# Performance work log

Measured on AMD Instinct MI355X. Metric: run time of the kernel, lower is better.

Reference implementation:

```python
import jax, jax.numpy as jnp
import numpy as np

N_NODES = 100000
N_EDGES = 1600000
IN_SIZE = 512
HID_SIZE = 256
OUT_SIZE = 40
K_STEPS = 10
ALPHA = 0.1


def setup_inputs() -> dict:
    key = jax.random.key(0)
    ks = jax.random.split(key, 8)
    features = jax.random.normal(ks[0], (N_NODES, IN_SIZE), dtype=jnp.float32)
    src = jax.random.randint(ks[1], (N_EDGES,), 0, N_NODES, dtype=jnp.int64)
    dst = jax.random.randint(ks[2], (N_EDGES,), 0, N_NODES, dtype=jnp.int64)
    # MLP params (Kaiming-ish scale)
    W1 = jax.random.normal(ks[3], (IN_SIZE, HID_SIZE), dtype=jnp.float32) / np.sqrt(IN_SIZE)
    b1 = jnp.zeros((HID_SIZE,), dtype=jnp.float32)
    W2 = jax.random.normal(ks[4], (HID_SIZE, OUT_SIZE), dtype=jnp.float32) / np.sqrt(HID_SIZE)
    b2 = jnp.zeros((OUT_SIZE,), dtype=jnp.float32)
    return {"features": features, "src": src, "dst": dst,
            "W1": W1, "b1": b1, "W2": W2, "b2": b2}


def reference(features, src, dst, W1, b1, W2, b2):
    # --- MLP encoder (dropout is identity in eval mode) ---
    h = jax.nn.relu(features @ W1 + b1)
    h = h @ W2 + b2  # [N, out_size]

    # --- Symmetric normalization (DGL APPNPConv, edge_weight=None) ---
    ones_e = jnp.ones((src.shape[0],), dtype=h.dtype)
    deg_out = jax.ops.segment_sum(ones_e, src, num_segments=N_NODES)
    deg_in = jax.ops.segment_sum(ones_e, dst, num_segments=N_NODES)
    norm_src = jnp.power(jnp.clip(deg_out, 1.0), -0.5)[:, None]  # D_out^{-1/2}
    norm_dst = jnp.power(jnp.clip(deg_in, 1.0), -0.5)[:, None]   # D_in^{-1/2}

    # --- k=10 APPNP propagation: h <- (1-a) * D^{-1/2} A D^{-1/2} h + a * h0 ---
    h0 = h

    def step(h, _):
        msg = (h * norm_src)[src]                                  # gather [E, out]
        agg = jax.ops.segment_sum(msg, dst, num_segments=N_NODES)  # scatter-add
        h = (1.0 - ALPHA) * (agg * norm_dst) + ALPHA * h0
        return h, None

    h, _ = jax.lax.scan(step, h, None, length=K_STEPS)
    return h
```

## Files before the change

### kernel.cpp

```cpp
#include <hip/hip_runtime.h>

#define N_NODES 100000
#define N_EDGES 1600000
#define IN_SIZE 512
#define HID_SIZE 256
#define OUT_SIZE 40
#define K_STEPS 10
#define ALPHA 0.1f
#define NP 100096

#define NCH 250
#define CH_E 6400
#define NBUK 391
#define NRS 8
#define HRS 12544
#define NCS 16
#define CS_E 100000

typedef _Float16 half8 __attribute__((ext_vector_type(8)));
typedef _Float16 half4 __attribute__((ext_vector_type(4)));
typedef float f32x4 __attribute__((ext_vector_type(4)));

struct __align__(8) Entry { int s; int d; };

__device__ inline void gld_lds16(const void* g, void* l) {
    __builtin_amdgcn_global_load_lds(
        (const __attribute__((address_space(1))) void*)g,
        (__attribute__((address_space(3))) void*)l,
        16, 0, 0);
}

__global__ __launch_bounds__(512) void hist_pass(const int* __restrict__ dst,
                                                 int* __restrict__ cnt) {
    __shared__ int h[NBUK];
    const int t = threadIdx.x, c = blockIdx.x;
    for (int j = t; j < NBUK; j += 512) h[j] = 0;
    __syncthreads();
    const int4* d4 = (const int4*)(dst + c * CH_E);
    for (int i = t; i < CH_E / 4; i += 512) {
        const int4 v = d4[i];
        atomicAdd(&h[v.x >> 8], 1);
        atomicAdd(&h[v.y >> 8], 1);
        atomicAdd(&h[v.z >> 8], 1);
        atomicAdd(&h[v.w >> 8], 1);
    }
    __syncthreads();
    for (int j = t; j < NBUK; j += 512) cnt[c * NBUK + j] = h[j];
}

__global__ __launch_bounds__(512) void bucket_scan(const int* __restrict__ cnt,
                                                   int* __restrict__ off,
                                                   int* __restrict__ boff) {
    __shared__ int tot[512];
    const int b = threadIdx.x;
    int s = 0;
    if (b < NBUK)
        for (int c = 0; c < NCH; ++c) s += cnt[c * NBUK + b];
    tot[b] = s;
    __syncthreads();
    for (int o = 1; o < 512; o <<= 1) {
        const int v = (b >= o) ? tot[b - o] : 0;
        __syncthreads();
        tot[b] += v;
        __syncthreads();
    }
    if (b < NBUK) {
        int run = tot[b] - s;
        boff[b] = run;
        for (int c = 0; c < NCH; ++c) { off[c * NBUK + b] = run; run += cnt[c * NBUK + b]; }
        if (b == NBUK - 1) boff[NBUK] = tot[b];
    }
}

__global__ __launch_bounds__(512) void scatter_pass(const int* __restrict__ src,
                                                    const int* __restrict__ dst,
                                                    const int* __restrict__ off,
                                                    Entry* __restrict__ ebuf) {
    __shared__ int cur[NBUK];
    const int t = threadIdx.x, c = blockIdx.x;
    for (int j = t; j < NBUK; j += 512) cur[j] = off[c * NBUK + j];
    __syncthreads();
    const int4* s4 = (const int4*)(src + c * CH_E);
    const int4* d4 = (const int4*)(dst + c * CH_E);
    for (int i = t; i < CH_E / 4; i += 512) {
        const int4 sv = s4[i];
        const int4 dv = d4[i];
        Entry e;
        int p;
        p = atomicAdd(&cur[dv.x >> 8], 1); e.s = sv.x; e.d = dv.x; ebuf[p] = e;
        p = atomicAdd(&cur[dv.y >> 8], 1); e.s = sv.y; e.d = dv.y; ebuf[p] = e;
        p = atomicAdd(&cur[dv.z >> 8], 1); e.s = sv.z; e.d = dv.z; ebuf[p] = e;
        p = atomicAdd(&cur[dv.w >> 8], 1); e.s = sv.w; e.d = dv.w; ebuf[p] = e;
    }
}

__global__ __launch_bounds__(256) void bucket_csr(const Entry* __restrict__ ebuf,
                                                  const int* __restrict__ boff,
                                                  int* __restrict__ rowp,
                                                  float* __restrict__ ndst,
                                                  int* __restrict__ csr) {
    __shared__ int hist[256];
    __shared__ int pref[256];
    __shared__ int cur[256];
    const int t = threadIdx.x, b = blockIdx.x;
    const int beg = boff[b], end = boff[b + 1];
    hist[t] = 0;
    __syncthreads();
    for (int i = beg + t; i < end; i += 256)
        atomicAdd(&hist[ebuf[i].d & 255], 1);
    __syncthreads();
    const int h = hist[t];
    pref[t] = h;
    __syncthreads();
    for (int o = 1; o < 256; o <<= 1) {
        const int v = (t >= o) ? pref[t - o] : 0;
        __syncthreads();
        pref[t] += v;
        __syncthreads();
    }
    const int val = beg + pref[t] - h;
    const int n = (b << 8) + t;
    if (n <= N_NODES) rowp[n] = val;
    if (n < N_NODES) ndst[n] = 1.0f / sqrtf((float)max(h, 1));
    cur[t] = val;
    __syncthreads();
    for (int i = beg + t; i < end; i += 256) {
        const Entry e = ebuf[i];
        const int pos = atomicAdd(&cur[e.d & 255], 1);
        csr[pos] = e.s;
    }
}

__global__ __launch_bounds__(512) void degsrc_part(const int* __restrict__ src,
                                                   int* __restrict__ partial) {
    __shared__ int h[HRS];
    const int t = threadIdx.x;
    const int r = blockIdx.x & (NRS - 1);
    const int c = blockIdx.x >> 3;
    const int base = r * HRS;
    for (int j = t; j < HRS; j += 512) h[j] = 0;
    __syncthreads();
    const int4* s4 = (const int4*)(src + (size_t)c * CS_E);
    for (int i = t; i < CS_E / 4; i += 512) {
        const int4 v = s4[i];
        unsigned u;
        u = (unsigned)(v.x - base); if (u < HRS) atomicAdd(&h[u], 1);
        u = (unsigned)(v.y - base); if (u < HRS) atomicAdd(&h[u], 1);
        u = (unsigned)(v.z - base); if (u < HRS) atomicAdd(&h[u], 1);
        u = (unsigned)(v.w - base); if (u < HRS) atomicAdd(&h[u], 1);
    }
    __syncthreads();
    for (int j = t; j < HRS; j += 512) partial[(size_t)c * (NRS * HRS) + base + j] = h[j];
}

__global__ __launch_bounds__(256) void nsrc_reduce(const int* __restrict__ partial,
                                                   float* __restrict__ nsrc) {
    const int n = blockIdx.x * 256 + threadIdx.x;
    int s = 0;
#pragma unroll
    for (int c = 0; c < NCS; ++c) s += partial[(size_t)c * (NRS * HRS) + n];
    if (n < N_NODES) nsrc[n] = 1.0f / sqrtf((float)max(s, 1));
}

__global__ __launch_bounds__(256) void prep_w1tp(const float* __restrict__ W1,
                                                 unsigned short* __restrict__ w1tp) {
    int idx = blockIdx.x * 256 + threadIdx.x;
    if (idx < IN_SIZE * HID_SIZE) {
        const int kt  = idx >> 14;
        const int p   = idx & 16383;
        const int n   = p >> 6;
        const int off = p & 63;
        const int j   = off & 7;
        const int ch  = (off >> 3) ^ (n & 7);
        const int kg  = kt * 64 + ch * 8 + j;
        _Float16 h = (_Float16)W1[(size_t)kg * HID_SIZE + n];
        w1tp[idx] = *(unsigned short*)&h;
    }
}

__global__ __launch_bounds__(512) void gemm1_f16(const float* __restrict__ X,
                                                 const unsigned short* __restrict__ w1tp,
                                                 const float* __restrict__ b1,
                                                 _Float16* __restrict__ h1t) {
    __shared__ __align__(16) _Float16 sA[128 * 64];
    __shared__ __align__(16) _Float16 sB[256 * 64];

    const int t    = threadIdx.x;
    const int lane = t & 63;
    const int w    = t >> 6;
    const int wr   = w >> 2;
    const int wc   = w & 3;
    const int n0   = blockIdx.x * 128;

    f32x4 acc[4][4];
#pragma unroll
    for (int i = 0; i < 4; ++i)
#pragma unroll
        for (int j = 0; j < 4; ++j) acc[i][j] = (f32x4)0.f;

    const int lo = lane & 15;
    const int hi = lane >> 4;
    const int l7 = lane & 7;

    for (int kk = 0; kk < IN_SIZE; kk += 64) {
        __syncthreads();
        {
            const unsigned short* gsrc = w1tp + ((size_t)(kk >> 6) << 14);
#pragma unroll
            for (int i = 0; i < 4; ++i) {
                const int c = t + i * 512;
                gld_lds16(gsrc + c * 8, &sB[c * 8]);
            }
        }
#pragma unroll
        for (int i = 0; i < 2; ++i) {
            int id  = t + i * 512;
            int row = id >> 3;
            int ch  = id & 7;
            int gr  = n0 + row;
            float4 x0 = make_float4(0.f, 0.f, 0.f, 0.f), x1 = x0;
            if (gr < N_NODES) {
                const float* p = X + (size_t)gr * IN_SIZE + kk + ch * 8;
                x0 = ((const float4*)p)[0];
                x1 = ((const float4*)p)[1];
            }
            half8 hv;
            hv[0] = (_Float16)x0.x; hv[1] = (_Float16)x0.y;
            hv[2] = (_Float16)x0.z; hv[3] = (_Float16)x0.w;
            hv[4] = (_Float16)x1.x; hv[5] = (_Float16)x1.y;
            hv[6] = (_Float16)x1.z; hv[7] = (_Float16)x1.w;
            *(half8*)&sA[row * 64 + ((ch ^ (row & 7)) << 3)] = hv;
        }
        __syncthreads();
#pragma unroll
        for (int s = 0; s < 2; ++s) {
            const int chs = ((s * 4 + hi) ^ l7) << 3;
            half8 af[4], bf[4];
#pragma unroll
            for (int f = 0; f < 4; ++f)
                af[f] = *(const half8*)&sA[(wr * 64 + f * 16 + lo) * 64 + chs];
#pragma unroll
            for (int f = 0; f < 4; ++f)
                bf[f] = *(const half8*)&sB[(wc * 64 + f * 16 + lo) * 64 + chs];
#pragma unroll
            for (int fi = 0; fi < 4; ++fi)
#pragma unroll
                for (int fj = 0; fj < 4; ++fj)
                    acc[fi][fj] = __builtin_amdgcn_mfma_f32_16x16x32_f16(
                        af[fi], bf[fj], acc[fi][fj], 0, 0, 0);
        }
    }

    float b1v[4];
#pragma unroll
    for (int fj = 0; fj < 4; ++fj) b1v[fj] = b1[wc * 64 + fj * 16 + lo];
#pragma unroll
    for (int fi = 0; fi < 4; ++fi) {
        const int nb = n0 + wr * 64 + fi * 16 + hi * 4;
#pragma unroll
        for (int fj = 0; fj < 4; ++fj) {
            const int c = wc * 64 + fj * 16 + lo;
            half4 hv;
#pragma unroll
            for (int r = 0; r < 4; ++r)
                hv[r] = (_Float16)fmaxf(acc[fi][fj][r] + b1v[fj], 0.f);
            *(half4*)(h1t + (size_t)c * NP + nb) = hv;
        }
    }
}

__global__ __launch_bounds__(256) void gemm2t(const _Float16* __restrict__ h1t,
                                              const float* __restrict__ W2,
                                              const float* __restrict__ b2,
                                              float* __restrict__ h0) {
    __shared__ float sW2[HID_SIZE * OUT_SIZE];
    const int t = threadIdx.x;
    const int n = blockIdx.x * 256 + t;
    for (int i = t; i < HID_SIZE * OUT_SIZE; i += 256) sW2[i] = W2[i];
    __syncthreads();

    float acc[OUT_SIZE];
#pragma unroll
    for (int o = 0; o < OUT_SIZE; ++o) acc[o] = b2[o];

    const _Float16* hp = h1t + n;
#pragma unroll 4
    for (int c = 0; c < HID_SIZE; ++c) {
        const float hv = (float)hp[(size_t)c * NP];
        const float* wrow = &sW2[c * OUT_SIZE];
#pragma unroll
        for (int o = 0; o < OUT_SIZE; ++o)
            acc[o] = fmaf(hv, wrow[o], acc[o]);
    }

    if (n < N_NODES) {
        float* dst = h0 + (size_t)n * OUT_SIZE;
#pragma unroll
        for (int o = 0; o < OUT_SIZE; o += 4)
            *(f32x4*)(dst + o) = *(f32x4*)&acc[o];
    }
}

__global__ __launch_bounds__(320) void g0_init(const float* __restrict__ h0,
                                               const float* __restrict__ nsrc,
                                               _Float16* __restrict__ g) {
    const int tid = threadIdx.x;
    const int ln  = tid / 5;
    const int q   = tid - ln * 5;
    const int n   = blockIdx.x * 64 + ln;
    if (n >= N_NODES) return;
    const float ns = nsrc[n];
    const f32x4 a = *(const f32x4*)(h0 + (size_t)n * OUT_SIZE + q * 8);
    const f32x4 b = *(const f32x4*)(h0 + (size_t)n * OUT_SIZE + q * 8 + 4);
    half8 gv;
    gv[0] = (_Float16)(ns * a[0]); gv[1] = (_Float16)(ns * a[1]);
    gv[2] = (_Float16)(ns * a[2]); gv[3] = (_Float16)(ns * a[3]);
    gv[4] = (_Float16)(ns * b[0]); gv[5] = (_Float16)(ns * b[1]);
    gv[6] = (_Float16)(ns * b[2]); gv[7] = (_Float16)(ns * b[3]);
    *(half8*)(g + (size_t)n * 64 + q * 8) = gv;
}

__global__ __launch_bounds__(320) void appnp_step3(const _Float16* __restrict__ gin,
                                                   const float* __restrict__ h0,
                                                   const int* __restrict__ rowp,
                                                   const int* __restrict__ csr,
                                                   const float* __restrict__ nsrc,
                                                   const float* __restrict__ ndst,
                                                   _Float16* __restrict__ gout,
                                                   float* __restrict__ hout,
                                                   int last) {
    const int tid = threadIdx.x;
    const int ln  = tid / 5;
    const int q   = tid - ln * 5;
    const int n   = blockIdx.x * 64 + ln;
    if (n >= N_NODES) return;

    const int beg = rowp[n];
    const int end = rowp[n + 1];
    const _Float16* gq = gin + q * 8;

    float acc[8];
#pragma unroll
    for (int j = 0; j < 8; ++j) acc[j] = 0.f;

    int e = beg;
    for (; e + 4 <= end; e += 4) {
        const int s0 = csr[e + 0];
        const int s1 = csr[e + 1];
        const int s2 = csr[e + 2];
        const int s3 = csr[e + 3];
        const half8 v0 = *(const half8*)(gq + (size_t)s0 * 64);
        const half8 v1 = *(const half8*)(gq + (size_t)s1 * 64);
        const half8 v2 = *(const half8*)(gq + (size_t)s2 * 64);
        const half8 v3 = *(const half8*)(gq + (size_t)s3 * 64);
#pragma unroll
        for (int j = 0; j < 8; ++j)
            acc[j] += (float)v0[j] + (float)v1[j] + (float)v2[j] + (float)v3[j];
    }
    for (; e < end; ++e) {
        const int s0 = csr[e];
        const half8 v0 = *(const half8*)(gq + (size_t)s0 * 64);
#pragma unroll
        for (int j = 0; j < 8; ++j) acc[j] += (float)v0[j];
    }

    const float nd = (1.0f - ALPHA) * ndst[n];
    const f32x4 h0a = *(const f32x4*)(h0 + (size_t)n * OUT_SIZE + q * 8);
    const f32x4 h0b = *(const f32x4*)(h0 + (size_t)n * OUT_SIZE + q * 8 + 4);
    float r[8];
    r[0] = nd * acc[0] + ALPHA * h0a[0]; r[1] = nd * acc[1] + ALPHA * h0a[1];
    r[2] = nd * acc[2] + ALPHA * h0a[2]; r[3] = nd * acc[3] + ALPHA * h0a[3];
    r[4] = nd * acc[4] + ALPHA * h0b[0]; r[5] = nd * acc[5] + ALPHA * h0b[1];
    r[6] = nd * acc[6] + ALPHA * h0b[2]; r[7] = nd * acc[7] + ALPHA * h0b[3];

    if (last) {
        f32x4 ra, rb;
        ra[0] = r[0]; ra[1] = r[1]; ra[2] = r[2]; ra[3] = r[3];
        rb[0] = r[4]; rb[1] = r[5]; rb[2] = r[6]; rb[3] = r[7];
        *(f32x4*)(hout + (size_t)n * OUT_SIZE + q * 8) = ra;
        *(f32x4*)(hout + (size_t)n * OUT_SIZE + q * 8 + 4) = rb;
    } else {
        const float ns = nsrc[n];
        half8 gv;
#pragma unroll
        for (int j = 0; j < 8; ++j) gv[j] = (_Float16)(ns * r[j]);
        *(half8*)(gout + (size_t)n * 64 + q * 8) = gv;
    }
}

extern "C" void kernel_launch(void* const* d_in, const int* in_sizes, int n_in,
                              void* d_out, int out_size, void* d_ws, size_t ws_size,
                              hipStream_t stream) {
    const float* X   = (const float*)d_in[0];
    const int*   src = (const int*)d_in[1];
    const int*   dst = (const int*)d_in[2];
    const float* W1  = (const float*)d_in[3];
    const float* b1  = (const float*)d_in[4];
    const float* W2  = (const float*)d_in[5];
    const float* b2  = (const float*)d_in[6];
    float* out = (float*)d_out;

    char* ws = (char*)d_ws;
    size_t off = 0;
    auto alloc = [&](size_t bytes) -> void* {
        void* p = ws + off;
        off = (off + bytes + 255) & ~(size_t)255;
        return p;
    };
    float* h0 = (float*)alloc((size_t)N_NODES * OUT_SIZE * 4);
    const size_t mark = off;

    unsigned short* w1tp = (unsigned short*)alloc((size_t)IN_SIZE * HID_SIZE * 2);
    _Float16*       h1t  = (_Float16*)alloc((size_t)HID_SIZE * NP * 2);

    off = mark;
    _Float16* gA = (_Float16*)alloc((size_t)N_NODES * 64 * 2);
    _Float16* gB = (_Float16*)alloc((size_t)N_NODES * 64 * 2);
    int*   partial = (int*)gA;
    Entry* ebuf    = (Entry*)gB;
    float* nsrc = (float*)alloc((size_t)N_NODES * 4);
    float* ndst = (float*)alloc((size_t)N_NODES * 4);
    int* rowp   = (int*)alloc((size_t)(N_NODES + 2) * 4);
    int* csr    = (int*)alloc((size_t)N_EDGES * 4);
    int* cnt    = (int*)alloc((size_t)NCH * NBUK * 4);
    int* offb   = (int*)alloc((size_t)NCH * NBUK * 4);
    int* boff   = (int*)alloc((size_t)(NBUK + 1) * 4);

    const int pgrid = (N_NODES + 63) / 64;
    const int ngrid256 = (N_NODES + 255) / 256;

    prep_w1tp<<<(IN_SIZE * HID_SIZE + 255) / 256, 256, 0, stream>>>(W1, w1tp);
    gemm1_f16<<<(N_NODES + 127) / 128, 512, 0, stream>>>(X, w1tp, b1, h1t);
    gemm2t<<<ngrid256, 256, 0, stream>>>(h1t, W2, b2, h0);

    hist_pass<<<NCH, 512, 0, stream>>>(dst, cnt);
    bucket_scan<<<1, 512, 0, stream>>>(cnt, offb, boff);
    scatter_pass<<<NCH, 512, 0, stream>>>(src, dst, offb, ebuf);
    bucket_csr<<<NBUK, 256, 0, stream>>>(ebuf, boff, rowp, ndst, csr);

    degsrc_part<<<NRS * NCS, 512, 0, stream>>>(src, partial);
    nsrc_reduce<<<(NRS * HRS) / 256, 256, 0, stream>>>(partial, nsrc);

    g0_init<<<pgrid, 320, 0, stream>>>(h0, nsrc, gA);

    const _Float16* gin = gA;
    for (int s = 0; s < K_STEPS; ++s) {
        const int last = (s == K_STEPS - 1) ? 1 : 0;
        _Float16* gout = (s & 1) ? gA : gB;
        appnp_step3<<<pgrid, 320, 0, stream>>>(gin, h0, rowp, csr, nsrc, ndst,
                                               gout, out, last);
        gin = gout;
    }
}
```

Measured before the change: 556.3 us.

## Fuse MLP second layer and g0 init into first GEMM kernel via MFMA

The first GEMM now keeps its ReLU hidden tile in LDS and computes the 256->40 second layer with f16 MFMA against a padded, transposed f16 W2, then writes h0 and the nsrc-scaled f16 g0 directly. This removes the h1t round-trip through global memory and the separate gemm2t and g0_init launches. The graph-preprocessing buffers no longer alias gA/gB, so the workspace grows, and the kernel adds extra barriers plus an f16 cast of W2.

Measured after the change: 478.3 us. -14.0%, faster.

```diff
diff --git a/kernel.cpp b/kernel.cpp
--- a/kernel.cpp
+++ b/kernel.cpp
@@ -7,7 +7,6 @@
 #define OUT_SIZE 40
 #define K_STEPS 10
 #define ALPHA 0.1f
-#define NP 100096
 
 #define NCH 250
 #define CH_E 6400
@@ -18,8 +17,8 @@
 #define CS_E 100000
 
 typedef _Float16 half8 __attribute__((ext_vector_type(8)));
-typedef _Float16 half4 __attribute__((ext_vector_type(4)));
 typedef float f32x4 __attribute__((ext_vector_type(4)));
+typedef float f32x2 __attribute__((ext_vector_type(2)));
 
 struct __align__(8) Entry { int s; int d; };
 
@@ -162,8 +161,10 @@
     if (n < N_NODES) nsrc[n] = 1.0f / sqrtf((float)max(s, 1));
 }
 
-__global__ __launch_bounds__(256) void prep_w1tp(const float* __restrict__ W1,
-                                                 unsigned short* __restrict__ w1tp) {
+__global__ __launch_bounds__(256) void prep_w(const float* __restrict__ W1,
+                                              const float* __restrict__ W2,
+                                              unsigned short* __restrict__ w1tp,
+                                              unsigned short* __restrict__ w2t) {
     int idx = blockIdx.x * 256 + threadIdx.x;
     if (idx < IN_SIZE * HID_SIZE) {
         const int kt  = idx >> 14;
@@ -175,15 +176,29 @@
         const int kg  = kt * 64 + ch * 8 + j;
         _Float16 h = (_Float16)W1[(size_t)kg * HID_SIZE + n];
         w1tp[idx] = *(unsigned short*)&h;
-    }
-}
-
-__global__ __launch_bounds__(512) void gemm1_f16(const float* __restrict__ X,
-                                                 const unsigned short* __restrict__ w1tp,
-                                                 const float* __restrict__ b1,
-                                                 _Float16* __restrict__ h1t) {
-    __shared__ __align__(16) _Float16 sA[128 * 64];
-    __shared__ __align__(16) _Float16 sB[256 * 64];
+    } else if (idx < IN_SIZE * HID_SIZE + 48 * HID_SIZE) {
+        const int i2 = idx - IN_SIZE * HID_SIZE;
+        const int o  = i2 >> 8;
+        const int c  = i2 & 255;
+        const float v = (o < OUT_SIZE) ? W2[(size_t)c * OUT_SIZE + o] : 0.f;
+        _Float16 h = (_Float16)v;
+        w2t[i2] = *(unsigned short*)&h;
+    }
+}
+
+__global__ __launch_bounds__(512) void gemm_fused(const float* __restrict__ X,
+                                                  const unsigned short* __restrict__ w1tp,
+                                                  const float* __restrict__ b1,
+                                                  const unsigned short* __restrict__ w2t,
+                                                  const float* __restrict__ b2,
+                                                  const float* __restrict__ nsrc,
+                                                  float* __restrict__ h0,
+                                                  _Float16* __restrict__ g0) {
+    __shared__ __align__(16) unsigned char lds[49152];
+    _Float16* sA = (_Float16*)lds;
+    _Float16* sB = sA + 128 * 64;
+    _Float16* sC = (_Float16*)lds;
+    _Float16* sW = sC + 128 * 72;
 
     const int t    = threadIdx.x;
     const int lane = t & 63;
@@ -254,70 +269,99 @@
     float b1v[4];
 #pragma unroll
     for (int fj = 0; fj < 4; ++fj) b1v[fj] = b1[wc * 64 + fj * 16 + lo];
-#pragma unroll
-    for (int fi = 0; fi < 4; ++fi) {
-        const int nb = n0 + wr * 64 + fi * 16 + hi * 4;
-#pragma unroll
-        for (int fj = 0; fj < 4; ++fj) {
-            const int c = wc * 64 + fj * 16 + lo;
-            half4 hv;
-#pragma unroll
-            for (int r = 0; r < 4; ++r)
-                hv[r] = (_Float16)fmaxf(acc[fi][fj][r] + b1v[fj], 0.f);
-            *(half4*)(h1t + (size_t)c * NP + nb) = hv;
-        }
-    }
-}
-
-__global__ __launch_bounds__(256) void gemm2t(const _Float16* __restrict__ h1t,
-                                              const float* __restrict__ W2,
-                                              const float* __restrict__ b2,
-                                              float* __restrict__ h0) {
-    __shared__ float sW2[HID_SIZE * OUT_SIZE];
-    const int t = threadIdx.x;
-    const int n = blockIdx.x * 256 + t;
-    for (int i = t; i < HID_SIZE * OUT_SIZE; i += 256) sW2[i] = W2[i];
-    __syncthreads();
-
-    float acc[OUT_SIZE];
-#pragma unroll
-    for (int o = 0; o < OUT_SIZE; ++o) acc[o] = b2[o];
-
-    const _Float16* hp = h1t + n;
-#pragma unroll 4
-    for (int c = 0; c < HID_SIZE; ++c) {
-        const float hv = (float)hp[(size_t)c * NP];
-        const float* wrow = &sW2[c * OUT_SIZE];
-#pragma unroll
-        for (int o = 0; o < OUT_SIZE; ++o)
-            acc[o] = fmaf(hv, wrow[o], acc[o]);
-    }
-
-    if (n < N_NODES) {
-        float* dst = h0 + (size_t)n * OUT_SIZE;
-#pragma unroll
-        for (int o = 0; o < OUT_SIZE; o += 4)
-            *(f32x4*)(dst + o) = *(f32x4*)&acc[o];
-    }
-}
-
-__global__ __launch_bounds__(320) void g0_init(const float* __restrict__ h0,
-                                               const float* __restrict__ nsrc,
-                                               _Float16* __restrict__ g) {
-    const int tid = threadIdx.x;
-    const int ln  = tid / 5;
-    const int q   = tid - ln * 5;
-    const int n   = blockIdx.x * 64 + ln;
-    if (n >= N_NODES) return;
-    const float ns = nsrc[n];
-    const f32x4 a = *(const f32x4*)(h0 + (size_t)n * OUT_SIZE + q * 8);
-    const f32x4 b = *(const f32x4*)(h0 + (size_t)n * OUT_SIZE + q * 8 + 4);
-    half8 gv;
-    gv[0] = (_Float16)(ns * a[0]); gv[1] = (_Float16)(ns * a[1]);
-    gv[2] = (_Float16)(ns * a[2]); gv[3] = (_Float16)(ns * a[3]);
-    gv[4] = (_Float16)(ns * b[0]); gv[5] = (_Float16)(ns * b[1]);
-    gv[6] = (_Float16)(ns * b[2]); gv[7] = (_Float16)(ns * b[3]);
-    *(half8*)(g + (size_t)n * 64 + q * 8) = gv;
+
+    __syncthreads();
+#pragma unroll
+    for (int i = 0; i < 3; ++i) {
+        const int id = t + i * 512;
+        const int o  = id >> 5;
+        const int ch = id & 31;
+        const uint4 v = *(const uint4*)(w2t + (size_t)o * HID_SIZE + ch * 8);
+        *(uint4*)&sW[o * 264 + ch * 8] = v;
+    }
+
+    f32x4 acc2[3];
+#pragma unroll
+    for (int f = 0; f < 3; ++f) acc2[f] = (f32x4)0.f;
+    float b2v[3];
+#pragma unroll
+    for (int f = 0; f < 3; ++f) {
+        const int o = f * 16 + lo;
+        b2v[f] = (o < OUT_SIZE) ? b2[o] : 0.f;
+    }
+
+    for (int j = 0; j < 4; ++j) {
+        if (j) __syncthreads();
+        if (wc == j) {
+#pragma unroll
+            for (int fi = 0; fi < 4; ++fi)
+#pragma unroll
+                for (int fj = 0; fj < 4; ++fj)
+#pragma unroll
+                    for (int r = 0; r < 4; ++r) {
+                        const int rl = wr * 64 + fi * 16 + hi * 4 + r;
+                        const int cl = fj * 16 + lo;
+                        const float v = fmaxf(acc[fi][fj][r] + b1v[fj], 0.f);
+                        sC[rl * 72 + cl] = (_Float16)v;
+                    }
+        }
+        __syncthreads();
+#pragma unroll
+        for (int ks = 0; ks < 2; ++ks) {
+            const half8 a = *(const half8*)&sC[(w * 16 + lo) * 72 + ks * 32 + hi * 8];
+#pragma unroll
+            for (int f = 0; f < 3; ++f) {
+                const half8 b = *(const half8*)&sW[(f * 16 + lo) * 264 + j * 64 + ks * 32 + hi * 8];
+                acc2[f] = __builtin_amdgcn_mfma_f32_16x16x32_f16(a, b, acc2[f], 0, 0, 0);
+            }
+        }
+    }
+
+    __syncthreads();
+    float* sOut = (float*)lds;
+#pragma unroll
+    for (int f = 0; f < 3; ++f) {
+        const int o = f * 16 + lo;
+#pragma unroll
+        for (int r = 0; r < 4; ++r) {
+            const int row = w * 16 + hi * 4 + r;
+            if (o < OUT_SIZE) sOut[row * OUT_SIZE + o] = acc2[f][r] + b2v[f];
+        }
+    }
+    __syncthreads();
+
+    const int nvalid = min(128, N_NODES - n0);
+    {
+        const int fcount = nvalid * OUT_SIZE;
+#pragma unroll
+        for (int i = 0; i < 5; ++i) {
+            const int idx = t + i * 512;
+            if (idx * 2 < fcount) {
+                f32x2 v;
+                v[0] = sOut[idx * 2];
+                v[1] = sOut[idx * 2 + 1];
+                *(f32x2*)(h0 + (size_t)n0 * OUT_SIZE + idx * 2) = v;
+            }
+        }
+    }
+#pragma unroll
+    for (int i = 0; i < 2; ++i) {
+        const int idx = t + i * 512;
+        const int row = idx >> 3;
+        const int q   = idx & 7;
+        if (row < nvalid) {
+            const int n = n0 + row;
+            const float ns = nsrc[n];
+            half8 gv;
+#pragma unroll
+            for (int k = 0; k < 8; ++k) {
+                const int col = q * 8 + k;
+                const float v = (col < OUT_SIZE) ? ns * sOut[row * OUT_SIZE + col] : 0.f;
+                gv[k] = (_Float16)v;
+            }
+            *(half8*)(g0 + (size_t)n * 64 + q * 8) = gv;
+        }
+    }
 }
 
 __global__ __launch_bounds__(320) void appnp_step3(const _Float16* __restrict__ gin,
@@ -407,17 +451,11 @@
         off = (off + bytes + 255) & ~(size_t)255;
         return p;
     };
-    float* h0 = (float*)alloc((size_t)N_NODES * OUT_SIZE * 4);
-    const size_t mark = off;
-
-    unsigned short* w1tp = (unsigned short*)alloc((size_t)IN_SIZE * HID_SIZE * 2);
-    _Float16*       h1t  = (_Float16*)alloc((size_t)HID_SIZE * NP * 2);
-
-    off = mark;
+    float*    h0 = (float*)alloc((size_t)N_NODES * OUT_SIZE * 4);
     _Float16* gA = (_Float16*)alloc((size_t)N_NODES * 64 * 2);
     _Float16* gB = (_Float16*)alloc((size_t)N_NODES * 64 * 2);
-    int*   partial = (int*)gA;
-    Entry* ebuf    = (Entry*)gB;
+    Entry* ebuf    = (Entry*)alloc((size_t)N_EDGES * 8);
+    int*   partial = (int*)alloc((size_t)NCS * NRS * HRS * 4);
     float* nsrc = (float*)alloc((size_t)N_NODES * 4);
     float* ndst = (float*)alloc((size_t)N_NODES * 4);
     int* rowp   = (int*)alloc((size_t)(N_NODES + 2) * 4);
@@ -425,23 +463,22 @@
     int* cnt    = (int*)alloc((size_t)NCH * NBUK * 4);
     int* offb   = (int*)alloc((size_t)NCH * NBUK * 4);
     int* boff   = (int*)alloc((size_t)(NBUK + 1) * 4);
+    unsigned short* w1tp = (unsigned short*)alloc((size_t)IN_SIZE * HID_SIZE * 2);
+    unsigned short* w2t  = (unsigned short*)alloc((size_t)48 * HID_SIZE * 2);
 
     const int pgrid = (N_NODES + 63) / 64;
-    const int ngrid256 = (N_NODES + 255) / 256;
-
-    prep_w1tp<<<(IN_SIZE * HID_SIZE + 255) / 256, 256, 0, stream>>>(W1, w1tp);
-    gemm1_f16<<<(N_NODES + 127) / 128, 512, 0, stream>>>(X, w1tp, b1, h1t);
-    gemm2t<<<ngrid256, 256, 0, stream>>>(h1t, W2, b2, h0);
 
     hist_pass<<<NCH, 512, 0, stream>>>(dst, cnt);
     bucket_scan<<<1, 512, 0, stream>>>(cnt, offb, boff);
     scatter_pass<<<NCH, 512, 0, stream>>>(src, dst, offb, ebuf);
     bucket_csr<<<NBUK, 256, 0, stream>>>(ebuf, boff, rowp, ndst, csr);
-
     degsrc_part<<<NRS * NCS, 512, 0, stream>>>(src, partial);
     nsrc_reduce<<<(NRS * HRS) / 256, 256, 0, stream>>>(partial, nsrc);
 
-    g0_init<<<pgrid, 320, 0, stream>>>(h0, nsrc, gA);
+    const int wtotal = IN_SIZE * HID_SIZE + 48 * HID_SIZE;
+    prep_w<<<(wtotal + 255) / 256, 256, 0, stream>>>(W1, W2, w1tp, w2t);
+    gemm_fused<<<(N_NODES + 127) / 128, 512, 0, stream>>>(X, w1tp, b1, w2t, b2,
+                                                          nsrc, h0, gA);
 
     const _Float16* gin = gA;
     for (int s = 0; s < K_STEPS; ++s) {
```
